# Kernel optimization log

Measured on AMD Instinct MI355X. Metric: run time of the kernel, lower is better.

## Reference

```python
import jax, jax.numpy as jnp
import numpy as np

B, N, M, D = 16, 4096, 4096, 3


def setup_inputs() -> dict:
    key = jax.random.key(0)
    k1, k2 = jax.random.split(key)
    xyz1 = jax.random.normal(k1, (B, N, D), dtype=jnp.float32)
    xyz2 = jax.random.normal(k2, (B, M, D), dtype=jnp.float32)
    return {"xyz1": xyz1, "xyz2": xyz2}


def _chamfer(xyz1, xyz2):
    # Squared pairwise distances via ||a||^2 + ||b||^2 - 2 a.b  -> [B, N, M]
    s1 = jnp.sum(xyz1 * xyz1, axis=-1)                     # [B, N]
    s2 = jnp.sum(xyz2 * xyz2, axis=-1)                     # [B, M]
    cross = jnp.einsum("bnd,bmd->bnm", xyz1, xyz2)        # [B, N, M]
    d2 = s1[:, :, None] + s2[:, None, :] - 2.0 * cross
    d2 = jnp.maximum(d2, 0.0)  # guard tiny negatives from cancellation
    dist1 = jnp.min(d2, axis=2)  # nearest point in set2 for each point in set1, [B, N]
    dist2 = jnp.min(d2, axis=1)  # nearest point in set1 for each point in set2, [B, M]
    return dist1, dist2


def reference(xyz1, xyz2):
    return _chamfer(xyz1, xyz2)
```

## Files before the change

### kernel.cpp

```cpp
#include <hip/hip_runtime.h>

typedef _Float16 h8     __attribute__((ext_vector_type(8)));
typedef float    f32x16 __attribute__((ext_vector_type(16)));

#define BB      16
#define NPTS    4096
#define WAVES   4
#define RPW     64
#define RPB     (WAVES * RPW)
#define CSPLIT  2
#define COLS    (NPTS / CSPLIT)
#define CHUNK   256
#define NCHUNK  (COLS / CHUNK)
#define TPB     (WAVES * 64)

__global__ __launch_bounds__(256) void chamfer_init_out(float* __restrict__ out) {
    int i = blockIdx.x * 256 + threadIdx.x;
    out[i] = 3.0e38f;
}

__global__ __launch_bounds__(TPB, 4) void chamfer_mfma(
    const float* __restrict__ xyz1,
    const float* __restrict__ xyz2,
    float* __restrict__ out)
{
    __shared__ __align__(16) _Float16 sb[2][CHUNK * 16];

    const int tid  = threadIdx.x;
    const int lane = tid & 63;
    const int wv   = tid >> 6;
    const int rb   = blockIdx.x;
    const int b    = blockIdx.y;
    const int z    = blockIdx.z;
    const int dir  = z & 1;
    const int csp  = z >> 1;

    const float* qbase = (dir == 0 ? xyz1 : xyz2) + b * NPTS * 3;
    const float* dbase = (dir == 0 ? xyz2 : xyz1) + b * NPTS * 3 + csp * COLS * 3;

    h8 af[2];
#pragma unroll
    for (int rbi = 0; rbi < 2; ++rbi) {
        const int row = rb * RPB + wv * RPW + rbi * 32 + (lane & 31);
        float x = qbase[row * 3 + 0], y = qbase[row * 3 + 1], z2 = qbase[row * 3 + 2];
        float s = fmaf(x, x, fmaf(y, y, z2 * z2));
        _Float16 xh = (_Float16)x, yh = (_Float16)y, zh = (_Float16)z2;
        _Float16 xl = (_Float16)(x - (float)xh);
        _Float16 yl = (_Float16)(y - (float)yh);
        _Float16 zl = (_Float16)(z2 - (float)zh);
        _Float16 sh = (_Float16)s;
        _Float16 sl = (_Float16)(s - (float)sh);
        _Float16 one = (_Float16)1.0f, zero = (_Float16)0.0f;
        af[rbi] = (lane < 32) ? h8{xh, yh, zh, xh, yh, zh, xl, yl}
                              : h8{zl, sh, sl, one, one, zero, zero, zero};
    }

    const f32x16 Z = {};
    float rm[2][16];
#pragma unroll
    for (int rbi = 0; rbi < 2; ++rbi)
#pragma unroll
        for (int r = 0; r < 16; ++r) rm[rbi][r] = 3.0e38f;

    const int loff = ((lane >> 5) << 8) + (lane & 31) * 8;

    float vx, vy, vz;
    auto stage_load = [&](int ch) {
        const float* p = dbase + (ch * CHUNK + tid) * 3;
        vx = p[0]; vy = p[1]; vz = p[2];
    };
    auto stage_write = [&](int buf) {
        float s = fmaf(vx, vx, fmaf(vy, vy, vz * vz));
        _Float16 xh = (_Float16)vx, yh = (_Float16)vy, zh = (_Float16)vz;
        _Float16 m2xh = (_Float16)(-2.0f) * xh;
        _Float16 m2yh = (_Float16)(-2.0f) * yh;
        _Float16 m2zh = (_Float16)(-2.0f) * zh;
        _Float16 m2xl = (_Float16)(-2.0f * (vx - (float)xh));
        _Float16 m2yl = (_Float16)(-2.0f * (vy - (float)yh));
        _Float16 m2zl = (_Float16)(-2.0f * (vz - (float)zh));
        _Float16 sh = (_Float16)s;
        _Float16 sl = (_Float16)(s - (float)sh);
        _Float16 one = (_Float16)1.0f, zero = (_Float16)0.0f;
        int off = (tid >> 5) * 512 + (tid & 31) * 8;
        *(h8*)&sb[buf][off]       = h8{m2xh, m2yh, m2zh, m2xl, m2yl, m2zl, m2xh, m2yh};
        *(h8*)&sb[buf][off + 256] = h8{m2zh, one, one, sh, sl, zero, zero, zero};
    };

    auto sweep = [&](int buf) {
        const _Float16* base = &sb[buf][0];
#pragma unroll 1
        for (int t = 0; t < CHUNK / 32; t += 2) {
            h8 b0 = *(const h8*)(base + t * 512 + loff);
            h8 b1 = *(const h8*)(base + (t + 1) * 512 + loff);
#pragma unroll
            for (int rbi = 0; rbi < 2; ++rbi) {
                f32x16 a0 = __builtin_amdgcn_mfma_f32_32x32x16_f16(af[rbi], b0, Z, 0, 0, 0);
                f32x16 a1 = __builtin_amdgcn_mfma_f32_32x32x16_f16(af[rbi], b1, Z, 0, 0, 0);
#pragma unroll
                for (int r = 0; r < 16; ++r)
                    rm[rbi][r] = fminf(fminf(a0[r], a1[r]), rm[rbi][r]);
            }
        }
    };

    stage_load(0);
    stage_write(0);
    __syncthreads();
#pragma unroll 1
    for (int ch = 0; ch < NCHUNK; ++ch) {
        int buf = ch & 1;
        if (ch + 1 < NCHUNK) stage_load(ch + 1);
        sweep(buf);
        if (ch + 1 < NCHUNK) stage_write(buf ^ 1);
        __syncthreads();
    }

#pragma unroll
    for (int rbi = 0; rbi < 2; ++rbi)
#pragma unroll
        for (int r = 0; r < 16; ++r) {
            float m = rm[rbi][r];
            m = fminf(m, __shfl_xor(m, 1));
            m = fminf(m, __shfl_xor(m, 2));
            m = fminf(m, __shfl_xor(m, 4));
            m = fminf(m, __shfl_xor(m, 8));
            m = fminf(m, __shfl_xor(m, 16));
            rm[rbi][r] = m;
        }
    if ((lane & 31) == 0) {
        const int half = lane >> 5;
        int* o = (int*)out + dir * (BB * NPTS) + b * NPTS + rb * RPB + wv * RPW;
#pragma unroll
        for (int rbi = 0; rbi < 2; ++rbi)
#pragma unroll
            for (int r = 0; r < 16; ++r) {
                int rr = (r & 3) + 8 * (r >> 2) + 4 * half;
                float val = fmaxf(rm[rbi][r], 0.0f);
                atomicMin(o + rbi * 32 + rr, __float_as_int(val));
            }
    }
}

extern "C" void kernel_launch(void* const* d_in, const int* in_sizes, int n_in,
                              void* d_out, int out_size, void* d_ws, size_t ws_size,
                              hipStream_t stream) {
    const float* xyz1 = (const float*)d_in[0];
    const float* xyz2 = (const float*)d_in[1];
    float* out = (float*)d_out;

    hipLaunchKernelGGL(chamfer_init_out, dim3(2 * BB * NPTS / 256), dim3(256), 0, stream, out);

    dim3 grid(NPTS / RPB, BB, 2 * CSPLIT);
    hipLaunchKernelGGL(chamfer_mfma, grid, dim3(TPB), 0, stream, xyz1, xyz2, out);
}
```

Baseline: 34.07 us.

## Compute both chamfer directions from one distance tile pass

Instead of launching separate blocks for each direction, each block computes the distance tile once and derives both row minima (per-lane registers) and column minima (an in-register reduction over the MFMA output, a cross-half shuffle, and a per-wave LDS buffer). The aim is to halve the MFMA work and staging traffic. In exchange it adds a 16-wide reduction and an LDS store per tile, plus a 16KB column buffer that lowers occupancy. CSPLIT is doubled to keep the grid size the same.

```diff
diff --git a/kernel.cpp b/kernel.cpp
--- a/kernel.cpp
+++ b/kernel.cpp
@@ -8,7 +8,7 @@
 #define WAVES   4
 #define RPW     64
 #define RPB     (WAVES * RPW)
-#define CSPLIT  2
+#define CSPLIT  4
 #define COLS    (NPTS / CSPLIT)
 #define CHUNK   256
 #define NCHUNK  (COLS / CHUNK)
@@ -19,26 +19,33 @@
     out[i] = 3.0e38f;
 }
 
+__device__ __forceinline__ float vmin16(const f32x16& v) {
+    float a = fminf(fminf(v[0], v[1]), fminf(v[2], v[3]));
+    float b = fminf(fminf(v[4], v[5]), fminf(v[6], v[7]));
+    float c = fminf(fminf(v[8], v[9]), fminf(v[10], v[11]));
+    float d = fminf(fminf(v[12], v[13]), fminf(v[14], v[15]));
+    return fminf(fminf(a, b), fminf(c, d));
+}
+
 __global__ __launch_bounds__(TPB, 4) void chamfer_mfma(
     const float* __restrict__ xyz1,
     const float* __restrict__ xyz2,
     float* __restrict__ out)
 {
     __shared__ __align__(16) _Float16 sb[2][CHUNK * 16];
+    __shared__ float colw[WAVES][COLS];
 
     const int tid  = threadIdx.x;
     const int lane = tid & 63;
     const int wv   = tid >> 6;
     const int rb   = blockIdx.x;
     const int b    = blockIdx.y;
-    const int z    = blockIdx.z;
-    const int dir  = z & 1;
-    const int csp  = z >> 1;
+    const int csp  = blockIdx.z;
 
-    const float* qbase = (dir == 0 ? xyz1 : xyz2) + b * NPTS * 3;
-    const float* dbase = (dir == 0 ? xyz2 : xyz1) + b * NPTS * 3 + csp * COLS * 3;
+    const float* qbase = xyz1 + b * NPTS * 3;
+    const float* dbase = xyz2 + b * NPTS * 3 + csp * COLS * 3;
 
-    h8 af[2];
+    h8 af0, af1;
 #pragma unroll
     for (int rbi = 0; rbi < 2; ++rbi) {
         const int row = rb * RPB + wv * RPW + rbi * 32 + (lane & 31);
@@ -51,16 +58,17 @@
         _Float16 sh = (_Float16)s;
         _Float16 sl = (_Float16)(s - (float)sh);
         _Float16 one = (_Float16)1.0f, zero = (_Float16)0.0f;
-        af[rbi] = (lane < 32) ? h8{xh, yh, zh, xh, yh, zh, xl, yl}
-                              : h8{zl, sh, sl, one, one, zero, zero, zero};
+        h8 a = (lane < 32) ? h8{xh, yh, zh, xh, yh, zh, xl, yl}
+                           : h8{zl, sh, sl, one, one, zero, zero, zero};
+        if (rbi == 0) af0 = a; else af1 = a;
     }
 
+    for (int i = tid; i < WAVES * COLS; i += TPB) ((float*)colw)[i] = 3.0e38f;
+
     const f32x16 Z = {};
-    float rm[2][16];
+    float rm0[16], rm1[16];
 #pragma unroll
-    for (int rbi = 0; rbi < 2; ++rbi)
-#pragma unroll
-        for (int r = 0; r < 16; ++r) rm[rbi][r] = 3.0e38f;
+    for (int r = 0; r < 16; ++r) { rm0[r] = 3.0e38f; rm1[r] = 3.0e38f; }
 
     const int loff = ((lane >> 5) << 8) + (lane & 31) * 8;
 
@@ -86,20 +94,21 @@
         *(h8*)&sb[buf][off + 256] = h8{m2zh, one, one, sh, sl, zero, zero, zero};
     };
 
-    auto sweep = [&](int buf) {
+    auto sweep = [&](int buf, int ch) {
         const _Float16* base = &sb[buf][0];
 #pragma unroll 1
-        for (int t = 0; t < CHUNK / 32; t += 2) {
-            h8 b0 = *(const h8*)(base + t * 512 + loff);
-            h8 b1 = *(const h8*)(base + (t + 1) * 512 + loff);
+        for (int t = 0; t < CHUNK / 32; ++t) {
+            h8 bt = *(const h8*)(base + t * 512 + loff);
+            f32x16 c0 = __builtin_amdgcn_mfma_f32_32x32x16_f16(af0, bt, Z, 0, 0, 0);
+            f32x16 c1 = __builtin_amdgcn_mfma_f32_32x32x16_f16(af1, bt, Z, 0, 0, 0);
 #pragma unroll
-            for (int rbi = 0; rbi < 2; ++rbi) {
-                f32x16 a0 = __builtin_amdgcn_mfma_f32_32x32x16_f16(af[rbi], b0, Z, 0, 0, 0);
-                f32x16 a1 = __builtin_amdgcn_mfma_f32_32x32x16_f16(af[rbi], b1, Z, 0, 0, 0);
+            for (int r = 0; r < 16; ++r) rm0[r] = fminf(c0[r], rm0[r]);
 #pragma unroll
-                for (int r = 0; r < 16; ++r)
-                    rm[rbi][r] = fminf(fminf(a0[r], a1[r]), rm[rbi][r]);
-            }
+            for (int r = 0; r < 16; ++r) rm1[r] = fminf(c1[r], rm1[r]);
+            float p = fminf(vmin16(c0), vmin16(c1));
+            p = fminf(p, __shfl_xor(p, 32));
+            if (lane < 32)
+                colw[wv][ch * CHUNK + t * 32 + lane] = fmaxf(p, 0.0f);
         }
     };
 
@@ -110,34 +119,46 @@
     for (int ch = 0; ch < NCHUNK; ++ch) {
         int buf = ch & 1;
         if (ch + 1 < NCHUNK) stage_load(ch + 1);
-        sweep(buf);
+        sweep(buf, ch);
         if (ch + 1 < NCHUNK) stage_write(buf ^ 1);
         __syncthreads();
     }
 
 #pragma unroll
-    for (int rbi = 0; rbi < 2; ++rbi)
+    for (int r = 0; r < 16; ++r) {
+        float m = rm0[r];
+        m = fminf(m, __shfl_xor(m, 1));
+        m = fminf(m, __shfl_xor(m, 2));
+        m = fminf(m, __shfl_xor(m, 4));
+        m = fminf(m, __shfl_xor(m, 8));
+        m = fminf(m, __shfl_xor(m, 16));
+        rm0[r] = m;
+        float n = rm1[r];
+        n = fminf(n, __shfl_xor(n, 1));
+        n = fminf(n, __shfl_xor(n, 2));
+        n = fminf(n, __shfl_xor(n, 4));
+        n = fminf(n, __shfl_xor(n, 8));
+        n = fminf(n, __shfl_xor(n, 16));
+        rm1[r] = n;
+    }
+    if ((lane & 31) == 0) {
+        const int half = lane >> 5;
+        int* o = (int*)out + b * NPTS + rb * RPB + wv * RPW;
 #pragma unroll
         for (int r = 0; r < 16; ++r) {
-            float m = rm[rbi][r];
-            m = fminf(m, __shfl_xor(m, 1));
-            m = fminf(m, __shfl_xor(m, 2));
-            m = fminf(m, __shfl_xor(m, 4));
-            m = fminf(m, __shfl_xor(m, 8));
-            m = fminf(m, __shfl_xor(m, 16));
-            rm[rbi][r] = m;
+            int rr = (r & 3) + 8 * (r >> 2) + 4 * half;
+            atomicMin(o + rr,      __float_as_int(fmaxf(rm0[r], 0.0f)));
+            atomicMin(o + 32 + rr, __float_as_int(fmaxf(rm1[r], 0.0f)));
         }
-    if ((lane & 31) == 0) {
-        const int half = lane >> 5;
-        int* o = (int*)out + dir * (BB * NPTS) + b * NPTS + rb * RPB + wv * RPW;
+    }
+
+    int* o2 = (int*)out + BB * NPTS + b * NPTS + csp * COLS;
 #pragma unroll
-        for (int rbi = 0; rbi < 2; ++rbi)
-#pragma unroll
-            for (int r = 0; r < 16; ++r) {
-                int rr = (r & 3) + 8 * (r >> 2) + 4 * half;
-                float val = fmaxf(rm[rbi][r], 0.0f);
-                atomicMin(o + rbi * 32 + rr, __float_as_int(val));
-            }
+    for (int k = 0; k < COLS / TPB; ++k) {
+        int i = tid + k * TPB;
+        float m = fminf(fminf(colw[0][i], colw[1][i]),
+                        fminf(colw[2][i], colw[3][i]));
+        atomicMin(o2 + i, __float_as_int(m));
     }
 }
 
@@ -150,6 +171,6 @@
 
     hipLaunchKernelGGL(chamfer_init_out, dim3(2 * BB * NPTS / 256), dim3(256), 0, stream, out);
 
-    dim3 grid(NPTS / RPB, BB, 2 * CSPLIT);
+    dim3 grid(NPTS / RPB, BB, CSPLIT);
     hipLaunchKernelGGL(chamfer_mfma, grid, dim3(TPB), 0, stream, xyz1, xyz2, out);
 }
```

New measurement: 52.46 us. 1.54x slower.
